# Optimization experiments

Hardware: AMD Instinct MI355X
Metric: run time of the kernel (lower is better)

The kernel has to match this reference:

```python
import jax, jax.numpy as jnp
import numpy as np

BS, N, D_IN, D_OUT = 4, 512, 64, 64
TEMP = 1.0
POOL_K = 0.5
N_KEEP = max(int(N * POOL_K), 1)  # 256
BN_EPS = 1e-5


def setup_inputs() -> dict:
    key = jax.random.key(0)
    ks = jax.random.split(key, 12)
    xav = lambda k, shape: jax.random.normal(k, shape, jnp.float32) * np.sqrt(2.0 / sum(shape))
    return {
        "x": jax.random.normal(ks[0], (BS, N, D_IN), jnp.float32),
        "att_proj_w": xav(ks[1], (D_IN, D_OUT)),
        "att_proj_b": jnp.zeros((D_OUT,), jnp.float32),
        "att_weight": xav(ks[2], (D_OUT, 1))[:, 0],  # (D_OUT,)
        "pwa_w": xav(ks[3], (D_IN, D_OUT)),
        "pwa_b": jnp.zeros((D_OUT,), jnp.float32),
        "pwoa_w": xav(ks[4], (D_IN, D_OUT)),
        "pwoa_b": jnp.zeros((D_OUT,), jnp.float32),
        "bn_gamma": jnp.ones((D_OUT,), jnp.float32),
        "bn_beta": jnp.zeros((D_OUT,), jnp.float32),
        "bn_mean": jnp.zeros((D_OUT,), jnp.float32),
        "bn_var": jnp.ones((D_OUT,), jnp.float32),
        "pool_w": xav(ks[5], (D_OUT, 1))[:, 0],  # (D_OUT,)
        "pool_b": jnp.zeros((), jnp.float32),
    }


def reference(x, att_proj_w, att_proj_b, att_weight, pwa_w, pwa_b,
              pwoa_w, pwoa_b, bn_gamma, bn_beta, bn_mean, bn_var,
              pool_w, pool_b):
    # ---- GraphAttentionLayer (eval mode: dropout off, BN uses running stats) ----
    # pairwise node product: (bs, i, j, d)
    pair = x[:, :, None, :] * x[:, None, :, :]
    a = jnp.tanh(jnp.einsum('bijd,de->bije', pair, att_proj_w) + att_proj_b)
    scores = jnp.einsum('bije,e->bij', a, att_weight) / TEMP
    att = jax.nn.softmax(scores, axis=-1)  # torch softmax over dim=-2 of (bs,i,j,1) == j axis
    agg = jnp.einsum('bij,bjd->bid', att, x)
    h = (agg @ pwa_w + pwa_b) + (x @ pwoa_w + pwoa_b)
    h = (h - bn_mean) * jax.lax.rsqrt(bn_var + BN_EPS) * bn_gamma + bn_beta
    h = jax.nn.selu(h)
    # ---- GraphPool (eval: dropout off) ----
    s = jax.nn.sigmoid(h @ pool_w + pool_b)  # (bs, N)
    _, idx = jax.lax.top_k(s, N_KEEP)        # (bs, N_KEEP), sorted desc like torch.topk
    hs = h * s[..., None]
    out = jnp.take_along_axis(hs, idx[..., None], axis=1)  # (bs, N_KEEP, D_OUT)
    return out
```

## Files before the change

### kernel.cpp

```cpp
#include <hip/hip_runtime.h>
#include <hip/hip_bf16.h>
#include <math.h>

#define BSZ 4
#define NN 512
#define DD 64
#define NKEEP 256

typedef __attribute__((ext_vector_type(8))) short short8;
typedef __attribute__((ext_vector_type(4))) float f32x4;

__device__ __forceinline__ ushort f2bf_rne(float f) {
  union { float f; unsigned u; } v; v.f = f;
  unsigned r = v.u + 0x7fffu + ((v.u >> 16) & 1u);
  return (ushort)(r >> 16);
}
__device__ __forceinline__ float bf2f(ushort h) {
  union { unsigned u; float f; } v; v.u = ((unsigned)h) << 16;
  return v.f;
}
__device__ __forceinline__ float fast_tanh(float x) {
  float e = __builtin_amdgcn_exp2f(x * 2.8853900817779268f);
  float r = __builtin_amdgcn_rcpf(e + 1.0f);
  return 1.0f - 2.0f * r;
}

__global__ __launch_bounds__(256, 2) void k_score(
    const float* __restrict__ x, const float* __restrict__ apw,
    const float* __restrict__ apb, const float* __restrict__ aw,
    float* __restrict__ sTp) {
  __shared__ float Xi_s[16 * 64];
  __shared__ ushort Yh[8 * 16 * 64];
  __shared__ ushort Yl[8 * 16 * 64];

  const int t = threadIdx.x;
  const int w = t >> 6, l = t & 63;
  const int b = blockIdx.x / 160;
  const int rem = blockIdx.x % 160;
  const int eh = rem / 80;
  const int tid = rem % 80;
  int jq, it;
  if (tid < 8)        { jq = 0; it = tid; }
  else if (tid < 24)  { jq = 1; it = tid - 8; }
  else if (tid < 48)  { jq = 2; it = tid - 24; }
  else                { jq = 3; it = tid - 48; }
  const int i0 = it * 16;
  const int jb0 = jq * 128;
  const int eh32 = eh * 32;
  const bool fast = (jb0 >= i0 + 16);

  const float* xb = x + (size_t)b * NN * DD;
  const int j0 = jb0 + w * 32;
  const bool wave_active = (j0 + 32 > i0);

  {
    const int row = t >> 4, dq = (t & 15) * 4;
    *reinterpret_cast<float4*>(&Xi_s[row * 64 + dq]) =
        *reinterpret_cast<const float4*>(xb + (size_t)(i0 + row) * DD + dq);
  }

  short8 ah[2][2], al[2][2];
  if (wave_active) {
    const int g = l >> 4;
    #pragma unroll
    for (int jt = 0; jt < 2; ++jt) {
      const int j = j0 + jt * 16 + (l & 15);
      #pragma unroll
      for (int ks = 0; ks < 2; ++ks) {
        const float* xr = xb + (size_t)j * DD + ks * 32 + g * 8;
        float4 u0 = *reinterpret_cast<const float4*>(xr);
        float4 u1 = *reinterpret_cast<const float4*>(xr + 4);
        float vv[8] = {u0.x, u0.y, u0.z, u0.w, u1.x, u1.y, u1.z, u1.w};
        short8 hh, ll;
        #pragma unroll
        for (int qq = 0; qq < 8; ++qq) {
          ushort hq = f2bf_rne(vv[qq]);
          hh[qq] = (short)hq;
          ll[qq] = (short)f2bf_rne(vv[qq] - bf2f(hq));
        }
        ah[jt][ks] = hh; al[jt][ks] = ll;
      }
    }
  }

  const int p_e = t >> 5;
  const int q = t & 31;
  const int ih = (q >> 4) * 8;
  const int d0 = (q & 15) * 4;

  auto build = [&](int rnd) {
    const int e = eh32 + rnd * 8 + p_e;
    float wt[4];
    #pragma unroll
    for (int k = 0; k < 4; ++k) wt[k] = apw[(d0 + k) * 64 + e];
    #pragma unroll
    for (int i2 = 0; i2 < 8; ++i2) {
      const int i = ih + i2;
      float4 xv = *reinterpret_cast<const float4*>(&Xi_s[i * 64 + d0]);
      const float p0v = xv.x * wt[0], p1v = xv.y * wt[1];
      const float p2v = xv.z * wt[2], p3v = xv.w * wt[3];
      const ushort h0 = f2bf_rne(p0v), h1 = f2bf_rne(p1v);
      const ushort h2 = f2bf_rne(p2v), h3 = f2bf_rne(p3v);
      uint2 hw, lw;
      hw.x = (uint)h0 | ((uint)h1 << 16);
      hw.y = (uint)h2 | ((uint)h3 << 16);
      lw.x = (uint)f2bf_rne(p0v - bf2f(h0)) | ((uint)f2bf_rne(p1v - bf2f(h1)) << 16);
      lw.y = (uint)f2bf_rne(p2v - bf2f(h2)) | ((uint)f2bf_rne(p3v - bf2f(h3)) << 16);
      const int byteoff = (p_e * 2048 + (i * 64 + d0) * 2) ^ ((i & 7) << 4);
      *reinterpret_cast<uint2*>(reinterpret_cast<char*>(Yh) + byteoff) = hw;
      *reinterpret_cast<uint2*>(reinterpret_cast<char*>(Yl) + byteoff) = lw;
    }
  };

  f32x4 srews[2];
  srews[0] = (f32x4){0.f, 0.f, 0.f, 0.f};
  srews[1] = (f32x4){0.f, 0.f, 0.f, 0.f};

  __syncthreads();
  build(0);

  #pragma unroll 1
  for (int r = 0; r < 4; ++r) {
    __syncthreads();
    if (wave_active) {
      const char* Ph = reinterpret_cast<const char*>(Yh);
      const char* Pl = reinterpret_cast<const char*>(Yl);
      const int il = l & 15, g = l >> 4;
      #pragma unroll
      for (int p = 0; p < 8; ++p) {
        const int e = eh32 + r * 8 + p;
        short8 bh[2], bl[2];
        #pragma unroll
        for (int ks = 0; ks < 2; ++ks) {
          const int byteoff =
              (p * 2048 + (il * 64 + ks * 32 + g * 8) * 2) ^ ((il & 7) << 4);
          bh[ks] = *reinterpret_cast<const short8*>(Ph + byteoff);
          bl[ks] = *reinterpret_cast<const short8*>(Pl + byteoff);
        }
        f32x4 acc[2];
        acc[0] = (f32x4){0.f, 0.f, 0.f, 0.f};
        acc[1] = (f32x4){0.f, 0.f, 0.f, 0.f};
        #pragma unroll
        for (int jt = 0; jt < 2; ++jt)
          #pragma unroll
          for (int ks = 0; ks < 2; ++ks) {
            acc[jt] = __builtin_amdgcn_mfma_f32_16x16x32_bf16(ah[jt][ks], bh[ks], acc[jt], 0, 0, 0);
            acc[jt] = __builtin_amdgcn_mfma_f32_16x16x32_bf16(ah[jt][ks], bl[ks], acc[jt], 0, 0, 0);
            acc[jt] = __builtin_amdgcn_mfma_f32_16x16x32_bf16(al[jt][ks], bh[ks], acc[jt], 0, 0, 0);
          }
        const float bias = apb[e], awv = aw[e];
        #pragma unroll
        for (int jt = 0; jt < 2; ++jt)
          #pragma unroll
          for (int rr = 0; rr < 4; ++rr)
            srews[jt][rr] += awv * fast_tanh(acc[jt][rr] + bias);
      }
    }
    __syncthreads();
    if (r < 3) build(r + 1);
  }

  float* plane = sTp + ((size_t)(eh * 4 + b)) * NN * NN;
  const int il = l & 15, g = l >> 4;
  const int iv = i0 + il;
  if (fast) {
    #pragma unroll
    for (int jt = 0; jt < 2; ++jt)
      #pragma unroll
      for (int rr = 0; rr < 4; ++rr)
        plane[(size_t)(j0 + jt * 16 + g * 4 + rr) * NN + iv] = srews[jt][rr];
    float* T = reinterpret_cast<float*>(Yh);
    #pragma unroll
    for (int jt = 0; jt < 2; ++jt)
      #pragma unroll
      for (int rr = 0; rr < 4; ++rr) {
        const int colw = w * 32 + jt * 16 + g * 4 + rr;
        const int byteoff = ((il * 128 + colw) * 4) ^ ((il & 7) << 4);
        *reinterpret_cast<float*>(reinterpret_cast<char*>(T) + byteoff) =
            srews[jt][rr];
      }
    __syncthreads();
    const int row = t >> 4, cb = (t & 15) * 8;
    const char* Tc = reinterpret_cast<const char*>(T);
    const int base = (row * 128 + cb) * 4;
    const int sw = (row & 7) << 4;
    f32x4 v0 = *reinterpret_cast<const f32x4*>(Tc + ((base) ^ sw));
    f32x4 v1 = *reinterpret_cast<const f32x4*>(Tc + ((base + 16) ^ sw));
    *reinterpret_cast<f32x4*>(plane + (size_t)(i0 + row) * NN + jb0 + cb) = v0;
    *reinterpret_cast<f32x4*>(plane + (size_t)(i0 + row) * NN + jb0 + cb + 4) = v1;
  } else if (wave_active) {
    #pragma unroll
    for (int jt = 0; jt < 2; ++jt)
      #pragma unroll
      for (int rr = 0; rr < 4; ++rr) {
        const int jv = j0 + jt * 16 + g * 4 + rr;
        const float v = srews[jt][rr];
        if (jv >= iv) plane[(size_t)iv * NN + jv] = v;
        if (jv > iv) plane[(size_t)jv * NN + iv] = v;
      }
  }
}

__global__ __launch_bounds__(256) void k_soft(
    const float* __restrict__ x, const float* __restrict__ sTp,
    const float* __restrict__ pwa, const float* __restrict__ pwab,
    const float* __restrict__ pwoa, const float* __restrict__ pwob,
    const float* __restrict__ gam, const float* __restrict__ bet,
    const float* __restrict__ mu, const float* __restrict__ var,
    const float* __restrict__ poolw, const float* __restrict__ poolb,
    float* __restrict__ h, float* __restrict__ s) {
  __shared__ float ssc[2][512];
  __shared__ float srm[2][4], srs[2][4];
  __shared__ float sagg[4][2][64];
  __shared__ float rag[2][64], xis[2][64];

  const int t = threadIdx.x;
  const int w = t >> 6, l = t & 63;
  const int b = blockIdx.x >> 8;
  const int rp = blockIdx.x & 255;
  const int i_r0 = rp * 2, i_r1 = i_r0 + 1;
  const float* xb = x + (size_t)b * NN * DD;
  const float* pl0 = sTp + (size_t)b * NN * NN;
  const float* pl1 = sTp + (size_t)(4 + b) * NN * NN;
  const int jw = w * 128;

  const size_t o0 = (size_t)i_r0 * NN + jw + l;
  const size_t o1 = (size_t)i_r1 * NN + jw + l;
  float r0a = pl0[o0] + pl1[o0];
  float r0b = pl0[o0 + 64] + pl1[o0 + 64];
  float r1a = pl0[o1] + pl1[o1];
  float r1b = pl0[o1 + 64] + pl1[o1 + 64];
  float m0 = fmaxf(r0a, r0b), m1 = fmaxf(r1a, r1b);
  #pragma unroll
  for (int off = 32; off; off >>= 1) {
    m0 = fmaxf(m0, __shfl_xor(m0, off, 64));
    m1 = fmaxf(m1, __shfl_xor(m1, off, 64));
  }
  if (l == 0) { srm[0][w] = m0; srm[1][w] = m1; }
  __syncthreads();
  m0 = fmaxf(fmaxf(srm[0][0], srm[0][1]), fmaxf(srm[0][2], srm[0][3]));
  m1 = fmaxf(fmaxf(srm[1][0], srm[1][1]), fmaxf(srm[1][2], srm[1][3]));

  const float L2E = 1.4426950408889634f;
  float e0a = __builtin_amdgcn_exp2f((r0a - m0) * L2E);
  float e0b = __builtin_amdgcn_exp2f((r0b - m0) * L2E);
  float e1a = __builtin_amdgcn_exp2f((r1a - m1) * L2E);
  float e1b = __builtin_amdgcn_exp2f((r1b - m1) * L2E);
  float ps0 = e0a + e0b, ps1 = e1a + e1b;
  #pragma unroll
  for (int off = 32; off; off >>= 1) {
    ps0 += __shfl_xor(ps0, off, 64);
    ps1 += __shfl_xor(ps1, off, 64);
  }
  if (l == 0) { srs[0][w] = ps0; srs[1][w] = ps1; }
  __syncthreads();
  const float inv0 = 1.f / (srs[0][0] + srs[0][1] + srs[0][2] + srs[0][3]);
  const float inv1 = 1.f / (srs[1][0] + srs[1][1] + srs[1][2] + srs[1][3]);
  ssc[0][jw + l] = e0a * inv0;
  ssc[0][jw + 64 + l] = e0b * inv0;
  ssc[1][jw + l] = e1a * inv1;
  ssc[1][jw + 64 + l] = e1b * inv1;
  __syncthreads();

  float g0 = 0.f, g1 = 0.f;
  #pragma unroll 4
  for (int jj = 0; jj < 128; ++jj) {
    const int j = jw + jj;
    const float xv = xb[(size_t)j * DD + l];
    g0 = fmaf(ssc[0][j], xv, g0);
    g1 = fmaf(ssc[1][j], xv, g1);
  }
  sagg[w][0][l] = g0;
  sagg[w][1][l] = g1;
  __syncthreads();

  if (w < 2) {
    const int irow = i_r0 + w;
    rag[w][l] = sagg[0][w][l] + sagg[1][w][l] + sagg[2][w][l] + sagg[3][w][l];
    xis[w][l] = xb[(size_t)irow * DD + l];
    float acc = 0.f;
    #pragma unroll 8
    for (int d = 0; d < 64; ++d) {
      acc = fmaf(rag[w][d], pwa[d * 64 + l], acc);
      acc = fmaf(xis[w][d], pwoa[d * 64 + l], acc);
    }
    acc += pwab[l] + pwob[l];
    float hb = (acc - mu[l]) * rsqrtf(var[l] + 1e-5f) * gam[l] + bet[l];
    const float SC = 1.0507009873554805f, AL = 1.6732632423543772f;
    float hv = hb > 0.f ? SC * hb : SC * AL * expm1f(hb);
    h[((size_t)(b * NN + irow)) * DD + l] = hv;

    float p = hv * poolw[l];
    #pragma unroll
    for (int off = 32; off; off >>= 1) p += __shfl_xor(p, off, 64);
    if (l == 0) s[b * NN + irow] = 1.f / (1.f + expf(-(p + poolb[0])));
  }
}

__global__ __launch_bounds__(512) void k_topk(
    const float* __restrict__ s, const float* __restrict__ h,
    float* __restrict__ out) {
  __shared__ float sv[NN];
  __shared__ int inv[NKEEP];
  const int b = blockIdx.x, t = threadIdx.x;
  sv[t] = s[b * NN + t];
  __syncthreads();

  const float my = sv[t];
  int r = 0;
  #pragma unroll 4
  for (int j0 = 0; j0 < NN; j0 += 4) {
    float4 v = *reinterpret_cast<const float4*>(&sv[j0]);
    r += (v.x > my) || (v.x == my && (j0 + 0) < t);
    r += (v.y > my) || (v.y == my && (j0 + 1) < t);
    r += (v.z > my) || (v.z == my && (j0 + 2) < t);
    r += (v.w > my) || (v.w == my && (j0 + 3) < t);
  }
  if (r < NKEEP) inv[r] = t;
  __syncthreads();

  for (int pos = t; pos < NKEEP * DD; pos += 512) {
    const int kk = pos >> 6, d = pos & 63;
    const int i = inv[kk];
    out[((size_t)b * NKEEP + kk) * DD + d] =
        h[((size_t)b * NN + i) * DD + d] * sv[i];
  }
}

extern "C" void kernel_launch(void* const* d_in, const int* in_sizes, int n_in,
                              void* d_out, int out_size, void* d_ws, size_t ws_size,
                              hipStream_t stream) {
  const float* x     = (const float*)d_in[0];
  const float* apw   = (const float*)d_in[1];
  const float* apb   = (const float*)d_in[2];
  const float* aw    = (const float*)d_in[3];
  const float* pwa   = (const float*)d_in[4];
  const float* pwab  = (const float*)d_in[5];
  const float* pwoa  = (const float*)d_in[6];
  const float* pwob  = (const float*)d_in[7];
  const float* gam   = (const float*)d_in[8];
  const float* bet   = (const float*)d_in[9];
  const float* mu    = (const float*)d_in[10];
  const float* var   = (const float*)d_in[11];
  const float* poolw = (const float*)d_in[12];
  const float* poolb = (const float*)d_in[13];
  float* out = (float*)d_out;

  float* sTp = (float*)d_ws;
  float* h   = sTp + (size_t)2 * BSZ * NN * NN;
  float* s   = h + (size_t)BSZ * NN * DD;

  k_score<<<640, 256, 0, stream>>>(x, apw, apb, aw, sTp);
  k_soft<<<BSZ * 256, 256, 0, stream>>>(x, sTp, pwa, pwab, pwoa, pwob,
                                        gam, bet, mu, var, poolw, poolb, h, s);
  k_topk<<<BSZ, 512, 0, stream>>>(s, h, out);
}
```

Baseline: 69.18 us.

## Double-buffer score LDS tiles, split MFMA accumulators, and split topk into gather kernel

The score kernel now double-buffers the bf16 hi/lo product tiles in LDS, with four e-values per round over eight rounds. Each round builds the next buffer while the current one is consumed, which drops one barrier per round. It also prefetches the next B fragments and splits the MFMA accumulation into independent chains so consecutive MFMAs do not wait on each other. The softmax-aggregate loop uses two accumulators per output to shorten its dependency chain. Top-k now only writes indices and scores, and a new 64-block gather kernel does the output gather with float4 accesses, at the cost of an extra launch.

```diff
diff --git a/kernel.cpp b/kernel.cpp
--- a/kernel.cpp
+++ b/kernel.cpp
@@ -30,8 +30,8 @@
     const float* __restrict__ apb, const float* __restrict__ aw,
     float* __restrict__ sTp) {
   __shared__ float Xi_s[16 * 64];
-  __shared__ ushort Yh[8 * 16 * 64];
-  __shared__ ushort Yl[8 * 16 * 64];
+  __shared__ ushort Yh[2][4 * 16 * 64];
+  __shared__ ushort Yl[2][4 * 16 * 64];
 
   const int t = threadIdx.x;
   const int w = t >> 6, l = t & 63;
@@ -83,20 +83,17 @@
     }
   }
 
-  const int p_e = t >> 5;
-  const int q = t & 31;
-  const int ih = (q >> 4) * 8;
-  const int d0 = (q & 15) * 4;
-
-  auto build = [&](int rnd) {
-    const int e = eh32 + rnd * 8 + p_e;
+  const int bi_g = l >> 4;
+  const int bdq = (l & 15) * 4;
+  auto build = [&](int rnd, int bf) {
+    const int e = eh32 + rnd * 4 + w;
     float wt[4];
     #pragma unroll
-    for (int k = 0; k < 4; ++k) wt[k] = apw[(d0 + k) * 64 + e];
-    #pragma unroll
-    for (int i2 = 0; i2 < 8; ++i2) {
-      const int i = ih + i2;
-      float4 xv = *reinterpret_cast<const float4*>(&Xi_s[i * 64 + d0]);
+    for (int k = 0; k < 4; ++k) wt[k] = apw[(bdq + k) * 64 + e];
+    #pragma unroll
+    for (int i2 = 0; i2 < 4; ++i2) {
+      const int i = i2 * 4 + bi_g;
+      float4 xv = *reinterpret_cast<const float4*>(&Xi_s[i * 64 + bdq]);
       const float p0v = xv.x * wt[0], p1v = xv.y * wt[1];
       const float p2v = xv.z * wt[2], p3v = xv.w * wt[3];
       const ushort h0 = f2bf_rne(p0v), h1 = f2bf_rne(p1v);
@@ -106,62 +103,78 @@
       hw.y = (uint)h2 | ((uint)h3 << 16);
       lw.x = (uint)f2bf_rne(p0v - bf2f(h0)) | ((uint)f2bf_rne(p1v - bf2f(h1)) << 16);
       lw.y = (uint)f2bf_rne(p2v - bf2f(h2)) | ((uint)f2bf_rne(p3v - bf2f(h3)) << 16);
-      const int byteoff = (p_e * 2048 + (i * 64 + d0) * 2) ^ ((i & 7) << 4);
-      *reinterpret_cast<uint2*>(reinterpret_cast<char*>(Yh) + byteoff) = hw;
-      *reinterpret_cast<uint2*>(reinterpret_cast<char*>(Yl) + byteoff) = lw;
+      const int byteoff = (w * 2048 + (i * 64 + bdq) * 2) ^ ((i & 7) << 4);
+      *reinterpret_cast<uint2*>(reinterpret_cast<char*>(Yh[bf]) + byteoff) = hw;
+      *reinterpret_cast<uint2*>(reinterpret_cast<char*>(Yl[bf]) + byteoff) = lw;
     }
   };
+
+  const int il = l & 15, g = l >> 4;
+  const int fbyte0 = ((il * 64 + g * 8) * 2) ^ ((il & 7) << 4);
+  const int fbyte1 = ((il * 64 + 32 + g * 8) * 2) ^ ((il & 7) << 4);
 
   f32x4 srews[2];
   srews[0] = (f32x4){0.f, 0.f, 0.f, 0.f};
   srews[1] = (f32x4){0.f, 0.f, 0.f, 0.f};
 
   __syncthreads();
-  build(0);
+  build(0, 0);
 
   #pragma unroll 1
-  for (int r = 0; r < 4; ++r) {
+  for (int r = 0; r < 8; ++r) {
     __syncthreads();
+    const char* Ph = reinterpret_cast<const char*>(Yh[r & 1]);
+    const char* Pl = reinterpret_cast<const char*>(Yl[r & 1]);
+
+    short8 cbh0, cbh1, cbl0, cbl1;
     if (wave_active) {
-      const char* Ph = reinterpret_cast<const char*>(Yh);
-      const char* Pl = reinterpret_cast<const char*>(Yl);
-      const int il = l & 15, g = l >> 4;
-      #pragma unroll
-      for (int p = 0; p < 8; ++p) {
-        const int e = eh32 + r * 8 + p;
-        short8 bh[2], bl[2];
-        #pragma unroll
-        for (int ks = 0; ks < 2; ++ks) {
-          const int byteoff =
-              (p * 2048 + (il * 64 + ks * 32 + g * 8) * 2) ^ ((il & 7) << 4);
-          bh[ks] = *reinterpret_cast<const short8*>(Ph + byteoff);
-          bl[ks] = *reinterpret_cast<const short8*>(Pl + byteoff);
+      cbh0 = *reinterpret_cast<const short8*>(Ph + fbyte0);
+      cbh1 = *reinterpret_cast<const short8*>(Ph + fbyte1);
+      cbl0 = *reinterpret_cast<const short8*>(Pl + fbyte0);
+      cbl1 = *reinterpret_cast<const short8*>(Pl + fbyte1);
+    }
+    if (r < 7) build(r + 1, (r + 1) & 1);
+
+    if (wave_active) {
+      #pragma unroll
+      for (int p = 0; p < 4; ++p) {
+        short8 nbh0, nbh1, nbl0, nbl1;
+        if (p < 3) {
+          nbh0 = *reinterpret_cast<const short8*>(Ph + (p + 1) * 2048 + fbyte0);
+          nbh1 = *reinterpret_cast<const short8*>(Ph + (p + 1) * 2048 + fbyte1);
+          nbl0 = *reinterpret_cast<const short8*>(Pl + (p + 1) * 2048 + fbyte0);
+          nbl1 = *reinterpret_cast<const short8*>(Pl + (p + 1) * 2048 + fbyte1);
         }
-        f32x4 acc[2];
-        acc[0] = (f32x4){0.f, 0.f, 0.f, 0.f};
-        acc[1] = (f32x4){0.f, 0.f, 0.f, 0.f};
-        #pragma unroll
-        for (int jt = 0; jt < 2; ++jt)
-          #pragma unroll
-          for (int ks = 0; ks < 2; ++ks) {
-            acc[jt] = __builtin_amdgcn_mfma_f32_16x16x32_bf16(ah[jt][ks], bh[ks], acc[jt], 0, 0, 0);
-            acc[jt] = __builtin_amdgcn_mfma_f32_16x16x32_bf16(ah[jt][ks], bl[ks], acc[jt], 0, 0, 0);
-            acc[jt] = __builtin_amdgcn_mfma_f32_16x16x32_bf16(al[jt][ks], bh[ks], acc[jt], 0, 0, 0);
-          }
+        f32x4 a00 = (f32x4){0.f, 0.f, 0.f, 0.f};
+        f32x4 a01 = (f32x4){0.f, 0.f, 0.f, 0.f};
+        f32x4 a10 = (f32x4){0.f, 0.f, 0.f, 0.f};
+        f32x4 a11 = (f32x4){0.f, 0.f, 0.f, 0.f};
+        a00 = __builtin_amdgcn_mfma_f32_16x16x32_bf16(ah[0][0], cbh0, a00, 0, 0, 0);
+        a10 = __builtin_amdgcn_mfma_f32_16x16x32_bf16(ah[1][0], cbh0, a10, 0, 0, 0);
+        a01 = __builtin_amdgcn_mfma_f32_16x16x32_bf16(ah[0][1], cbh1, a01, 0, 0, 0);
+        a11 = __builtin_amdgcn_mfma_f32_16x16x32_bf16(ah[1][1], cbh1, a11, 0, 0, 0);
+        a00 = __builtin_amdgcn_mfma_f32_16x16x32_bf16(ah[0][0], cbl0, a00, 0, 0, 0);
+        a10 = __builtin_amdgcn_mfma_f32_16x16x32_bf16(ah[1][0], cbl0, a10, 0, 0, 0);
+        a01 = __builtin_amdgcn_mfma_f32_16x16x32_bf16(ah[0][1], cbl1, a01, 0, 0, 0);
+        a11 = __builtin_amdgcn_mfma_f32_16x16x32_bf16(ah[1][1], cbl1, a11, 0, 0, 0);
+        a00 = __builtin_amdgcn_mfma_f32_16x16x32_bf16(al[0][0], cbh0, a00, 0, 0, 0);
+        a10 = __builtin_amdgcn_mfma_f32_16x16x32_bf16(al[1][0], cbh0, a10, 0, 0, 0);
+        a01 = __builtin_amdgcn_mfma_f32_16x16x32_bf16(al[0][1], cbh1, a01, 0, 0, 0);
+        a11 = __builtin_amdgcn_mfma_f32_16x16x32_bf16(al[1][1], cbh1, a11, 0, 0, 0);
+
+        const int e = eh32 + r * 4 + p;
         const float bias = apb[e], awv = aw[e];
         #pragma unroll
-        for (int jt = 0; jt < 2; ++jt)
-          #pragma unroll
-          for (int rr = 0; rr < 4; ++rr)
-            srews[jt][rr] += awv * fast_tanh(acc[jt][rr] + bias);
+        for (int rr = 0; rr < 4; ++rr) {
+          srews[0][rr] += awv * fast_tanh(a00[rr] + a01[rr] + bias);
+          srews[1][rr] += awv * fast_tanh(a10[rr] + a11[rr] + bias);
+        }
+        cbh0 = nbh0; cbh1 = nbh1; cbl0 = nbl0; cbl1 = nbl1;
       }
     }
-    __syncthreads();
-    if (r < 3) build(r + 1);
   }
 
   float* plane = sTp + ((size_t)(eh * 4 + b)) * NN * NN;
-  const int il = l & 15, g = l >> 4;
   const int iv = i0 + il;
   if (fast) {
     #pragma unroll
@@ -169,7 +182,8 @@
       #pragma unroll
       for (int rr = 0; rr < 4; ++rr)
         plane[(size_t)(j0 + jt * 16 + g * 4 + rr) * NN + iv] = srews[jt][rr];
-    float* T = reinterpret_cast<float*>(Yh);
+    __syncthreads();
+    float* T = reinterpret_cast<float*>(Yh[0]);
     #pragma unroll
     for (int jt = 0; jt < 2; ++jt)
       #pragma unroll
@@ -262,16 +276,19 @@
   ssc[1][jw + 64 + l] = e1b * inv1;
   __syncthreads();
 
-  float g0 = 0.f, g1 = 0.f;
+  float g0a = 0.f, g0b = 0.f, g1a = 0.f, g1b = 0.f;
   #pragma unroll 4
-  for (int jj = 0; jj < 128; ++jj) {
+  for (int jj = 0; jj < 128; jj += 2) {
     const int j = jw + jj;
-    const float xv = xb[(size_t)j * DD + l];
-    g0 = fmaf(ssc[0][j], xv, g0);
-    g1 = fmaf(ssc[1][j], xv, g1);
-  }
-  sagg[w][0][l] = g0;
-  sagg[w][1][l] = g1;
+    const float xv0 = xb[(size_t)j * DD + l];
+    const float xv1 = xb[(size_t)(j + 1) * DD + l];
+    g0a = fmaf(ssc[0][j], xv0, g0a);
+    g1a = fmaf(ssc[1][j], xv0, g1a);
+    g0b = fmaf(ssc[0][j + 1], xv1, g0b);
+    g1b = fmaf(ssc[1][j + 1], xv1, g1b);
+  }
+  sagg[w][0][l] = g0a + g0b;
+  sagg[w][1][l] = g1a + g1b;
   __syncthreads();
 
   if (w < 2) {
@@ -298,10 +315,9 @@
 }
 
 __global__ __launch_bounds__(512) void k_topk(
-    const float* __restrict__ s, const float* __restrict__ h,
-    float* __restrict__ out) {
+    const float* __restrict__ s, int* __restrict__ invi,
+    float* __restrict__ sval) {
   __shared__ float sv[NN];
-  __shared__ int inv[NKEEP];
   const int b = blockIdx.x, t = threadIdx.x;
   sv[t] = s[b * NN + t];
   __syncthreads();
@@ -316,15 +332,21 @@
     r += (v.z > my) || (v.z == my && (j0 + 2) < t);
     r += (v.w > my) || (v.w == my && (j0 + 3) < t);
   }
-  if (r < NKEEP) inv[r] = t;
-  __syncthreads();
-
-  for (int pos = t; pos < NKEEP * DD; pos += 512) {
-    const int kk = pos >> 6, d = pos & 63;
-    const int i = inv[kk];
-    out[((size_t)b * NKEEP + kk) * DD + d] =
-        h[((size_t)b * NN + i) * DD + d] * sv[i];
-  }
+  if (r < NKEEP) { invi[b * NKEEP + r] = t; sval[b * NKEEP + r] = my; }
+}
+
+__global__ __launch_bounds__(256) void k_gather(
+    const int* __restrict__ invi, const float* __restrict__ sval,
+    const float* __restrict__ h, float* __restrict__ out) {
+  const int b = blockIdx.x >> 4, kg = blockIdx.x & 15;
+  const int t = threadIdx.x;
+  const int kk = kg * 16 + (t >> 4);
+  const int d4 = (t & 15) * 4;
+  const int i = invi[b * NKEEP + kk];
+  const float svv = sval[b * NKEEP + kk];
+  float4 v = *reinterpret_cast<const float4*>(h + ((size_t)(b * NN + i)) * DD + d4);
+  v.x *= svv; v.y *= svv; v.z *= svv; v.w *= svv;
+  *reinterpret_cast<float4*>(out + ((size_t)(b * NKEEP + kk)) * DD + d4) = v;
 }
 
 extern "C" void kernel_launch(void* const* d_in, const int* in_sizes, int n_in,
@@ -349,9 +371,12 @@
   float* sTp = (float*)d_ws;
   float* h   = sTp + (size_t)2 * BSZ * NN * NN;
   float* s   = h + (size_t)BSZ * NN * DD;
+  int* invi  = (int*)(s + BSZ * NN);
+  float* sval = (float*)(invi + BSZ * NKEEP);
 
   k_score<<<640, 256, 0, stream>>>(x, apw, apb, aw, sTp);
   k_soft<<<BSZ * 256, 256, 0, stream>>>(x, sTp, pwa, pwab, pwoa, pwob,
                                         gam, bet, mu, var, poolw, poolb, h, s);
-  k_topk<<<BSZ, 512, 0, stream>>>(s, h, out);
-}
+  k_topk<<<BSZ, 512, 0, stream>>>(s, invi, sval);
+  k_gather<<<BSZ * 16, 256, 0, stream>>>(invi, sval, h, out);
+}
```

Measured after the change: 70.34 us. No clear change (+1.7%).
